# Kernel optimization log

Hardware: AMD Instinct MI355X
Metric: run time of the kernel (lower is better)

## Reference

```python
import jax, jax.numpy as jnp
import numpy as np

# Per-type input feature dims (NODE_DIM values); max dim = 128 = padded width of x.
NODE_DIMS = np.array([16, 32, 64, 128, 64, 32, 16, 128], dtype=np.int32)
N_TYPES = 8
MAX_DIM = 128
FEAT = 256          # node_feature_dim
N_GRAPHS = 100000   # batch_size; one node of each type per graph


def setup_inputs() -> dict:
    key = jax.random.key(0)
    k1, k2, k3 = jax.random.split(key, 3)
    num_nodes = N_GRAPHS * N_TYPES
    x = jax.random.normal(k1, (num_nodes, MAX_DIM), dtype=jnp.float32)
    # Per-type Linear weights, padded to MAX_DIM on the input axis.
    W = jax.random.normal(k2, (N_TYPES, FEAT, MAX_DIM), dtype=jnp.float32) * 0.05
    b = jax.random.normal(k3, (N_TYPES, FEAT), dtype=jnp.float32) * 0.05
    return {"x": x, "W": W, "b": b}


def reference(x, W, b):
    # Node n = g*N_TYPES + k is the type-k node of graph g (the gather index
    # ptr[b] + node_name.index(k) in the original). Dropout is eval-mode (identity).
    # Mask weight columns beyond each type's true input dim: equivalent to
    # slicing x[:, :NODE_DIM[k]] before the per-type Linear.
    mask = (jnp.arange(MAX_DIM)[None, None, :] < jnp.asarray(NODE_DIMS)[:, None, None]).astype(x.dtype)  # [T,1,D]
    W_eff = W * mask  # [T,F,D]
    xg = x.reshape(N_GRAPHS, N_TYPES, MAX_DIM)  # [G,T,D]
    y = jnp.einsum("gtd,tfd->gtf", xg, W_eff) + b[None, :, :]  # [G,T,F]
    return y.reshape(N_GRAPHS * N_TYPES, FEAT)
```

## Files before the change

### kernel.cpp

```cpp
#include <hip/hip_runtime.h>
#include <hip/hip_bf16.h>

#define N_GRAPHS 100000
#define NT 8
#define MAXD 128
#define FEAT 256

typedef __attribute__((ext_vector_type(8))) short short8;
typedef __attribute__((ext_vector_type(4))) float f32x4;

__device__ __forceinline__ unsigned short f2bf(float f) {
    unsigned u = __builtin_bit_cast(unsigned, f);
    u = (u + 0x7fffu + ((u >> 16) & 1u)) >> 16;
    return (unsigned short)u;
}

template<int KS>
__global__ __launch_bounds__(256, 4)
void node_enc_kernel(const float* __restrict__ x,
                     const float* __restrict__ W,
                     const float* __restrict__ bias_g,
                     float* __restrict__ out,
                     int tmap, int dmap)
{
    constexpr int K32  = KS * 32;
    constexpr int ROWS = 128;
    const int t   = (tmap >> (8 * blockIdx.y)) & 0xff;
    const int dim = (dmap >> (8 * blockIdx.y)) & 0xff;
    const int tid  = threadIdx.x;
    const int lane = tid & 63;
    const int wave = tid >> 6;
    const int n0   = wave * 64;
    const int cgrp = lane >> 4;
    const int c16  = lane & 15;

    __shared__ unsigned short As[ROWS][K32 + 8];

    short8 Bf[KS][4];
    float bias[4];
    const float* Wt = W + (size_t)t * FEAT * MAXD;
    #pragma unroll
    for (int nt = 0; nt < 4; ++nt) {
        const int col = n0 + nt * 16 + c16;
        bias[nt] = bias_g[t * FEAT + col];
        #pragma unroll
        for (int ks = 0; ks < KS; ++ks) {
            const int k = ks * 32 + cgrp * 8;
            const float* wp = Wt + (size_t)col * MAXD + k;
            f32x4 w0 = *(const f32x4*)wp;
            f32x4 w1 = *(const f32x4*)(wp + 4);
            short8 s;
            #pragma unroll
            for (int j = 0; j < 4; ++j) {
                s[j]     = (k + j     < dim) ? (short)f2bf(w0[j]) : (short)0;
                s[j + 4] = (k + j + 4 < dim) ? (short)f2bf(w1[j]) : (short)0;
            }
            Bf[ks][nt] = s;
        }
    }

    const int grow0 = blockIdx.x * ROWS;

    {
        constexpr int TPR    = K32 / 8;
        constexpr int RPP    = 256 / TPR;
        constexpr int PASSES = ROWS / RPP;
        const int rloc = tid / TPR;
        const int kg   = tid % TPR;
        const bool kload = (kg * 8 < dim);
        #pragma unroll
        for (int p = 0; p < PASSES; ++p) {
            const int i = p * RPP + rloc;
            const int g = grow0 + i;
            f32x4 v0 = {0.f,0.f,0.f,0.f}, v1 = {0.f,0.f,0.f,0.f};
            if (kload && g < N_GRAPHS) {
                const float* rp = x + ((size_t)g * NT + t) * MAXD + kg * 8;
                v0 = __builtin_nontemporal_load((const f32x4*)rp);
                v1 = __builtin_nontemporal_load((const f32x4*)rp + 1);
            }
            short8 s;
            #pragma unroll
            for (int j = 0; j < 4; ++j) {
                s[j]     = (short)f2bf(v0[j]);
                s[j + 4] = (short)f2bf(v1[j]);
            }
            *(short8*)&As[i][kg * 8] = s;
        }
    }
    __syncthreads();

    const bool full = (grow0 + ROWS <= N_GRAPHS);

    #pragma unroll
    for (int ms = 0; ms < ROWS / 16; ++ms) {
        short8 a[KS];
        #pragma unroll
        for (int ks = 0; ks < KS; ++ks)
            a[ks] = *(const short8*)&As[ms * 16 + c16][ks * 32 + cgrp * 8];

        f32x4 acc[4] = {{0,0,0,0},{0,0,0,0},{0,0,0,0},{0,0,0,0}};
        #pragma unroll
        for (int ks = 0; ks < KS; ++ks) {
            #pragma unroll
            for (int nt = 0; nt < 4; ++nt)
                acc[nt] = __builtin_amdgcn_mfma_f32_16x16x32_bf16(a[ks], Bf[ks][nt], acc[nt], 0, 0, 0);
        }

        if (full) {
            #pragma unroll
            for (int nt = 0; nt < 4; ++nt) {
                const int col = n0 + nt * 16 + c16;
                #pragma unroll
                for (int r = 0; r < 4; ++r) {
                    const int g = grow0 + ms * 16 + cgrp * 4 + r;
                    __builtin_nontemporal_store(acc[nt][r] + bias[nt],
                        &out[((size_t)g * NT + t) * FEAT + col]);
                }
            }
        } else {
            #pragma unroll
            for (int nt = 0; nt < 4; ++nt) {
                const int col = n0 + nt * 16 + c16;
                #pragma unroll
                for (int r = 0; r < 4; ++r) {
                    const int g = grow0 + ms * 16 + cgrp * 4 + r;
                    if (g < N_GRAPHS)
                        __builtin_nontemporal_store(acc[nt][r] + bias[nt],
                            &out[((size_t)g * NT + t) * FEAT + col]);
                }
            }
        }
    }
}

extern "C" void kernel_launch(void* const* d_in, const int* in_sizes, int n_in,
                              void* d_out, int out_size, void* d_ws, size_t ws_size,
                              hipStream_t stream)
{
    const float* x = (const float*)d_in[0];
    const float* W = (const float*)d_in[1];
    const float* b = (const float*)d_in[2];
    float* out = (float*)d_out;

    const int chunks = (N_GRAPHS + 127) / 128;

    node_enc_kernel<1><<<dim3(chunks, 4), 256, 0, stream>>>(x, W, b, out,
        0 | (1 << 8) | (5 << 16) | (6 << 24),
        16 | (32 << 8) | (32 << 16) | (16 << 24));
    node_enc_kernel<2><<<dim3(chunks, 2), 256, 0, stream>>>(x, W, b, out,
        2 | (4 << 8), 64 | (64 << 8));
    node_enc_kernel<4><<<dim3(chunks, 2), 256, 0, stream>>>(x, W, b, out,
        3 | (7 << 8), 128 | (128 << 8));
}
```

Baseline: 339.8 us.

## Fuse per-type launches into one kernel with double-buffered staging and prepacked weights

Replaces the three per-dim-group launches with a single kernel in which each 64-row block walks all eight node types in sequence. The next type's x tile is staged into a second LDS buffer while the current type's MFMAs and stores run. Weights are converted to bf16 and masked once by a prepack kernel into workspace, so blocks load ready-made fragments instead of converting fp32 W per block. The price is an extra small kernel launch, a deep recursive template expansion with higher register pressure, and smaller row tiles.

```diff
diff --git a/kernel.cpp b/kernel.cpp
--- a/kernel.cpp
+++ b/kernel.cpp
@@ -2,101 +2,130 @@
 #include <hip/hip_bf16.h>
 
 #define N_GRAPHS 100000
-#define NT 8
+#define NTYPES 8
 #define MAXD 128
 #define FEAT 256
+#define ROWS 64
 
 typedef __attribute__((ext_vector_type(8))) short short8;
 typedef __attribute__((ext_vector_type(4))) float f32x4;
-
-__device__ __forceinline__ unsigned short f2bf(float f) {
+typedef __attribute__((ext_vector_type(4))) unsigned uint4v;
+
+constexpr int DIMS[NTYPES] = {16, 32, 64, 128, 64, 32, 16, 128};
+
+__device__ __forceinline__ unsigned f2bf_u(float f) {
     unsigned u = __builtin_bit_cast(unsigned, f);
-    u = (u + 0x7fffu + ((u >> 16) & 1u)) >> 16;
-    return (unsigned short)u;
-}
-
-template<int KS>
-__global__ __launch_bounds__(256, 4)
-void node_enc_kernel(const float* __restrict__ x,
-                     const float* __restrict__ W,
-                     const float* __restrict__ bias_g,
-                     float* __restrict__ out,
-                     int tmap, int dmap)
-{
-    constexpr int K32  = KS * 32;
-    constexpr int ROWS = 128;
-    const int t   = (tmap >> (8 * blockIdx.y)) & 0xff;
-    const int dim = (dmap >> (8 * blockIdx.y)) & 0xff;
-    const int tid  = threadIdx.x;
-    const int lane = tid & 63;
-    const int wave = tid >> 6;
+    return (u + 0x7fffu + ((u >> 16) & 1u)) >> 16;
+}
+__device__ __forceinline__ unsigned cvt2(float lo, float hi) {
+    return f2bf_u(lo) | (f2bf_u(hi) << 16);
+}
+__device__ __forceinline__ short8 cvt8(f32x4 a, f32x4 b) {
+    uint4v u;
+    u.x = cvt2(a.x, a.y); u.y = cvt2(a.z, a.w);
+    u.z = cvt2(b.x, b.y); u.w = cvt2(b.z, b.w);
+    return __builtin_bit_cast(short8, u);
+}
+
+__global__ __launch_bounds__(256)
+void prepack_w(const float* __restrict__ W, short8* __restrict__ wp)
+{
+    const int idx  = blockIdx.x * 256 + threadIdx.x;
+    const int c16  = idx & 15;
+    const int cgrp = (idx >> 4) & 3;
+    const int ks   = (idx >> 6) & 3;
+    const int nt   = (idx >> 8) & 3;
+    const int wb   = (idx >> 10) & 3;
+    const int t    = (idx >> 12) & 7;
+    const int col  = wb * 64 + nt * 16 + c16;
+    const int k    = ks * 32 + cgrp * 8;
+    const int dim  = 16 << ((0x30123210u >> (4 * t)) & 0xf);
+    const float* src = W + ((size_t)t * FEAT + col) * MAXD + k;
+    f32x4 a = *(const f32x4*)src;
+    f32x4 b = *(const f32x4*)(src + 4);
+    #pragma unroll
+    for (int j = 0; j < 4; ++j) {
+        if (k + j     >= dim) a[j] = 0.f;
+        if (k + 4 + j >= dim) b[j] = 0.f;
+    }
+    wp[idx] = cvt8(a, b);
+}
+
+template<int K32>
+__device__ __forceinline__ void stage_tile(const float* __restrict__ x, int grow0, int t,
+                                           unsigned short (* __restrict__ As)[136], int tid)
+{
+    constexpr int TPR    = K32 / 8;
+    constexpr int RPP    = 256 / TPR;
+    constexpr int PASSES = ROWS / RPP;
+    const int rloc = tid / TPR;
+    const int kg   = tid % TPR;
+    #pragma unroll
+    for (int p = 0; p < PASSES; ++p) {
+        const int i = p * RPP + rloc;
+        int g = grow0 + i;
+        if (g >= N_GRAPHS) g = N_GRAPHS - 1;
+        const float* rp = x + ((size_t)g * NTYPES + t) * MAXD + kg * 8;
+        f32x4 v0 = __builtin_nontemporal_load((const f32x4*)rp);
+        f32x4 v1 = __builtin_nontemporal_load((const f32x4*)rp + 1);
+        *(short8*)&As[i][kg * 8] = cvt8(v0, v1);
+    }
+}
+
+template<int T, bool PRE>
+__device__ __forceinline__ void type_step(const float* __restrict__ x,
+                                          const float* __restrict__ W,
+                                          const float* __restrict__ bias_g,
+                                          float* __restrict__ out,
+                                          const short8* __restrict__ wp,
+                                          unsigned short (* __restrict__ As)[ROWS][136],
+                                          int grow0, int tid, bool full)
+{
+    constexpr int DIM = DIMS[T];
+    constexpr int KS  = (DIM + 31) / 32;
+    const int lane = tid & 63, wave = tid >> 6;
+    const int cgrp = lane >> 4, c16 = lane & 15;
     const int n0   = wave * 64;
-    const int cgrp = lane >> 4;
-    const int c16  = lane & 15;
-
-    __shared__ unsigned short As[ROWS][K32 + 8];
 
     short8 Bf[KS][4];
-    float bias[4];
-    const float* Wt = W + (size_t)t * FEAT * MAXD;
+    float  bias[4];
     #pragma unroll
     for (int nt = 0; nt < 4; ++nt) {
-        const int col = n0 + nt * 16 + c16;
-        bias[nt] = bias_g[t * FEAT + col];
-        #pragma unroll
-        for (int ks = 0; ks < KS; ++ks) {
-            const int k = ks * 32 + cgrp * 8;
-            const float* wp = Wt + (size_t)col * MAXD + k;
-            f32x4 w0 = *(const f32x4*)wp;
-            f32x4 w1 = *(const f32x4*)(wp + 4);
-            short8 s;
-            #pragma unroll
-            for (int j = 0; j < 4; ++j) {
-                s[j]     = (k + j     < dim) ? (short)f2bf(w0[j]) : (short)0;
-                s[j + 4] = (k + j + 4 < dim) ? (short)f2bf(w1[j]) : (short)0;
+        bias[nt] = bias_g[T * FEAT + n0 + nt * 16 + c16];
+        if constexpr (PRE) {
+            #pragma unroll
+            for (int ks = 0; ks < KS; ++ks)
+                Bf[ks][nt] = wp[((((T * 4 + wave) * 4 + nt) * 4 + ks) * 4 + cgrp) * 16 + c16];
+        } else {
+            const int col = n0 + nt * 16 + c16;
+            #pragma unroll
+            for (int ks = 0; ks < KS; ++ks) {
+                const int k = ks * 32 + cgrp * 8;
+                const float* wpf = W + ((size_t)T * FEAT + col) * MAXD + k;
+                f32x4 w0 = *(const f32x4*)wpf;
+                f32x4 w1 = *(const f32x4*)(wpf + 4);
+                #pragma unroll
+                for (int j = 0; j < 4; ++j) {
+                    if (k + j     >= DIM) w0[j] = 0.f;
+                    if (k + 4 + j >= DIM) w1[j] = 0.f;
+                }
+                Bf[ks][nt] = cvt8(w0, w1);
             }
-            Bf[ks][nt] = s;
         }
     }
 
-    const int grow0 = blockIdx.x * ROWS;
-
-    {
-        constexpr int TPR    = K32 / 8;
-        constexpr int RPP    = 256 / TPR;
-        constexpr int PASSES = ROWS / RPP;
-        const int rloc = tid / TPR;
-        const int kg   = tid % TPR;
-        const bool kload = (kg * 8 < dim);
-        #pragma unroll
-        for (int p = 0; p < PASSES; ++p) {
-            const int i = p * RPP + rloc;
-            const int g = grow0 + i;
-            f32x4 v0 = {0.f,0.f,0.f,0.f}, v1 = {0.f,0.f,0.f,0.f};
-            if (kload && g < N_GRAPHS) {
-                const float* rp = x + ((size_t)g * NT + t) * MAXD + kg * 8;
-                v0 = __builtin_nontemporal_load((const f32x4*)rp);
-                v1 = __builtin_nontemporal_load((const f32x4*)rp + 1);
-            }
-            short8 s;
-            #pragma unroll
-            for (int j = 0; j < 4; ++j) {
-                s[j]     = (short)f2bf(v0[j]);
-                s[j + 4] = (short)f2bf(v1[j]);
-            }
-            *(short8*)&As[i][kg * 8] = s;
-        }
-    }
     __syncthreads();
 
-    const bool full = (grow0 + ROWS <= N_GRAPHS);
-
+    if constexpr (T + 1 < NTYPES)
+        stage_tile<((DIMS[T + 1] + 31) / 32) * 32>(x, grow0, T + 1, As[(T + 1) & 1], tid);
+
+    const unsigned short (* __restrict__ A)[136] = As[T & 1];
     #pragma unroll
     for (int ms = 0; ms < ROWS / 16; ++ms) {
         short8 a[KS];
         #pragma unroll
         for (int ks = 0; ks < KS; ++ks)
-            a[ks] = *(const short8*)&As[ms * 16 + c16][ks * 32 + cgrp * 8];
+            a[ks] = *(const short8*)&A[ms * 16 + c16][ks * 32 + cgrp * 8];
 
         f32x4 acc[4] = {{0,0,0,0},{0,0,0,0},{0,0,0,0},{0,0,0,0}};
         #pragma unroll
@@ -114,7 +143,7 @@
                 for (int r = 0; r < 4; ++r) {
                     const int g = grow0 + ms * 16 + cgrp * 4 + r;
                     __builtin_nontemporal_store(acc[nt][r] + bias[nt],
-                        &out[((size_t)g * NT + t) * FEAT + col]);
+                        &out[((size_t)g * NTYPES + T) * FEAT + col]);
                 }
             }
         } else {
@@ -126,11 +155,29 @@
                     const int g = grow0 + ms * 16 + cgrp * 4 + r;
                     if (g < N_GRAPHS)
                         __builtin_nontemporal_store(acc[nt][r] + bias[nt],
-                            &out[((size_t)g * NT + t) * FEAT + col]);
+                            &out[((size_t)g * NTYPES + T) * FEAT + col]);
                 }
             }
         }
     }
+
+    if constexpr (T + 1 < NTYPES)
+        type_step<T + 1, PRE>(x, W, bias_g, out, wp, As, grow0, tid, full);
+}
+
+template<bool PRE>
+__global__ __launch_bounds__(256, 4)
+void node_enc_fused(const float* __restrict__ x, const float* __restrict__ W,
+                    const float* __restrict__ bias_g, float* __restrict__ out,
+                    const short8* __restrict__ wp)
+{
+    __shared__ __align__(16) unsigned short As[2][ROWS][136];
+    const int tid   = threadIdx.x;
+    const int grow0 = blockIdx.x * ROWS;
+    const bool full = (grow0 + ROWS <= N_GRAPHS);
+
+    stage_tile<((DIMS[0] + 31) / 32) * 32>(x, grow0, 0, As[0], tid);
+    type_step<0, PRE>(x, W, bias_g, out, wp, As, grow0, tid, full);
 }
 
 extern "C" void kernel_launch(void* const* d_in, const int* in_sizes, int n_in,
@@ -142,13 +189,14 @@
     const float* b = (const float*)d_in[2];
     float* out = (float*)d_out;
 
-    const int chunks = (N_GRAPHS + 127) / 128;
-
-    node_enc_kernel<1><<<dim3(chunks, 4), 256, 0, stream>>>(x, W, b, out,
-        0 | (1 << 8) | (5 << 16) | (6 << 24),
-        16 | (32 << 8) | (32 << 16) | (16 << 24));
-    node_enc_kernel<2><<<dim3(chunks, 2), 256, 0, stream>>>(x, W, b, out,
-        2 | (4 << 8), 64 | (64 << 8));
-    node_enc_kernel<4><<<dim3(chunks, 2), 256, 0, stream>>>(x, W, b, out,
-        3 | (7 << 8), 128 | (128 << 8));
-}
+    const int chunks = (N_GRAPHS + ROWS - 1) / ROWS;
+    const size_t wp_bytes = (size_t)NTYPES * 4 * 4 * 4 * 4 * 16 * sizeof(short8);
+
+    if (ws_size >= wp_bytes) {
+        short8* wp = (short8*)d_ws;
+        prepack_w<<<128, 256, 0, stream>>>(W, wp);
+        node_enc_fused<true><<<chunks, 256, 0, stream>>>(x, W, b, out, wp);
+    } else {
+        node_enc_fused<false><<<chunks, 256, 0, stream>>>(x, W, b, out, nullptr);
+    }
+}
```

Measured after the change: 305.0 us. 10.3% less time.
